# Optimization experiments

Hardware: AMD Instinct MI355X
Metric: run time of the kernel (lower is better)

## Reference

```python
import jax, jax.numpy as jnp
import numpy as np

B, N, FIN, FOUT, OPD = 2048, 64, 96, 128, 48
EPS = 1e-5      # nn.LayerNorm default eps
SLOPE = 0.01    # F.leaky_relu default negative_slope (used in GAT forward)


def setup_inputs() -> dict:
    key = jax.random.key(0)
    ks = jax.random.split(key, 12)
    stdv = 1.0 / np.sqrt(FOUT)
    h = jax.random.normal(ks[0], (B, N, FIN), jnp.float32)
    # binary DAG-style adjacency (float mask, as used multiplicatively in torch)
    adj = (jax.random.uniform(ks[1], (B, N, N)) < 0.3).astype(jnp.float32)
    op_emb = jax.random.normal(ks[2], (B, N, OPD), jnp.float32)
    # DenseGraphFlow params (uniform(-stdv, stdv) per reset_parameters)
    W = jax.random.uniform(ks[3], (FIN, FOUT), jnp.float32, -stdv, stdv)
    b = jax.random.uniform(ks[4], (FOUT,), jnp.float32, -stdv, stdv)
    Wop_d = jax.random.normal(ks[5], (OPD, FOUT), jnp.float32) * 0.05
    bop_d = jnp.zeros((FOUT,), jnp.float32)
    # GraphAttentionLayer params
    Wk = jax.random.normal(ks[6], (FIN, FOUT), jnp.float32) * 0.05
    a_w = jax.random.normal(ks[7], (FOUT,), jnp.float32) * 0.05
    Wop_g = jax.random.normal(ks[8], (OPD, FOUT), jnp.float32) * 0.05
    bop_g = jnp.zeros((FOUT,), jnp.float32)
    gamma = jnp.ones((FOUT,), jnp.float32)
    beta = jnp.zeros((FOUT,), jnp.float32)
    return dict(h=h, adj=adj, op_emb=op_emb, W=W, b=b, Wop_d=Wop_d, bop_d=bop_d,
                Wk=Wk, a_w=a_w, Wop_g=Wop_g, bop_g=bop_g, gamma=gamma, beta=beta)


def reference(h, adj, op_emb, W, b, Wop_d, bop_d, Wk, a_w, Wop_g, bop_g, gamma, beta):
    # ---- DenseGraphFlow (residual=True, opattention=True) ----
    support = jnp.einsum('bnf,fo->bno', h, W)                       # [B,N,FOUT]
    gate_d = jax.nn.sigmoid(op_emb @ Wop_d + bop_d)                 # [B,N,FOUT]
    dense = gate_d * jnp.einsum('bij,bjo->bio', adj, support) + support + b

    # ---- GraphAttentionLayer (unique_attn_proj=False -> Wq=Wv=Wk) ----
    Whk = jnp.einsum('bnf,fo->bno', h, Wk)                          # [B,N,FOUT]
    # torch builds a_input[b,i,j,m] = Whk[b,j,m] * Whk[b,i,m], then projects with
    # a (Linear FOUT->1). Exactly equivalent factored form (no [B,N,N,F] tensor):
    scores = jnp.einsum('bim,bjm->bij', Whk * a_w, Whk)             # [B,N,N]
    alpha = jnp.where(scores >= 0, scores, SLOPE * scores) * adj    # leaky_relu then adj mask
    attn = jax.nn.softmax(alpha, axis=-1)                           # softmax over j (torch dim=-2 of [b,i,j,1])
    hp = jnp.einsum('bij,bjo->bio', attn, Whk)                      # aggregate values
    gate_g = jax.nn.sigmoid(op_emb @ Wop_g + bop_g)
    hp = gate_g * hp
    # LayerNorm over last dim
    mu = jnp.mean(hp, axis=-1, keepdims=True)
    var = jnp.var(hp, axis=-1, keepdims=True)
    hp = (hp - mu) / jnp.sqrt(var + EPS) * gamma + beta

    # ---- ensemble combine ----
    return (dense + hp) / 2
```

## Files before the change

kernel.cpp:

```cpp
#include <hip/hip_runtime.h>

#define NB 2048
#define NN 64
#define KFIN 96
#define KFOUT 128
#define KOPD 48

typedef __attribute__((ext_vector_type(8))) short bf8;
typedef __attribute__((ext_vector_type(4))) float f32x4;
typedef __attribute__((ext_vector_type(4))) unsigned short us4;

__device__ __forceinline__ unsigned short f2bf(float f) {
  unsigned int u = __builtin_bit_cast(unsigned int, f);
  u += 0x7fffu + ((u >> 16) & 1u);
  return (unsigned short)(u >> 16);
}
__device__ __forceinline__ float bf2f(unsigned short s) {
  unsigned int u = ((unsigned int)s) << 16;
  return __builtin_bit_cast(float, u);
}
__device__ __forceinline__ us4 pack4(float a, float b, float c, float d) {
  us4 q; q.x = f2bf(a); q.y = f2bf(b); q.z = f2bf(c); q.w = f2bf(d); return q;
}

__global__ void prep_weights(const float* __restrict__ W, const float* __restrict__ Wk,
                             const float* __restrict__ Wd, const float* __restrict__ Wg,
                             unsigned short* __restrict__ ws) {
  int idx = blockIdx.x * 256 + threadIdx.x;
  if (idx >= 40960) return;
  float v;
  if (idx < 12288)      { int o = idx / 96, f = idx % 96; v = W[f * 128 + o]; }
  else if (idx < 24576) { int r = idx - 12288; int o = r / 96, f = r % 96; v = Wk[f * 128 + o]; }
  else if (idx < 32768) { int r = idx - 24576; int o = r >> 6, k = r & 63; v = (k < 48) ? Wd[k * 128 + o] : 0.f; }
  else                  { int r = idx - 32768; int o = r >> 6, k = r & 63; v = (k < 48) ? Wg[k * 128 + o] : 0.f; }
  ws[idx] = f2bf(v);
}

__global__ __launch_bounds__(256, 2) void gin_fused(
    const float* __restrict__ hg, const float* __restrict__ adjg,
    const float* __restrict__ opeg, const float* __restrict__ bvec,
    const float* __restrict__ bopd, const float* __restrict__ bopg,
    const float* __restrict__ awv, const float* __restrict__ gmv,
    const float* __restrict__ btv, const unsigned short* __restrict__ ws,
    float* __restrict__ out) {
  __shared__ __align__(16) char smem[50176];
  unsigned short* h_s   = (unsigned short*)smem;
  unsigned short* ope_s = (unsigned short*)(smem + 13312);
  unsigned short* adj_s = (unsigned short*)(smem + 22528);
  unsigned short* supT  = (unsigned short*)(smem + 31744);
  unsigned short* whkT  = (unsigned short*)smem;
  unsigned short* whk   = supT;

  const int t  = threadIdx.x;
  const int b  = blockIdx.x;
  const int w  = t >> 6;
  const int l  = t & 63;
  const int lr = l & 15;
  const int lg = l >> 4;
  const int kcol = 8 * lg;
  const int arow = w * 16 + lr;

  {
    const float4* p = (const float4*)(hg + (size_t)b * (NN * KFIN));
    #pragma unroll
    for (int i = 0; i < 6; ++i) {
      int idx = t + i * 256;
      float4 v = p[idx];
      int e = idx * 4, r = e / 96, c = e - r * 96;
      *(us4*)(h_s + r * 104 + c) = pack4(v.x, v.y, v.z, v.w);
    }
    const float4* pa = (const float4*)(adjg + (size_t)b * (NN * NN));
    #pragma unroll
    for (int i = 0; i < 4; ++i) {
      int idx = t + i * 256;
      float4 v = pa[idx];
      int e = idx * 4, r = e >> 6, c = e & 63;
      *(us4*)(adj_s + r * 72 + c) = pack4(v.x, v.y, v.z, v.w);
    }
    const float4* po = (const float4*)(opeg + (size_t)b * (NN * KOPD));
    #pragma unroll
    for (int i = 0; i < 3; ++i) {
      int idx = t + i * 256;
      float4 v = po[idx];
      int e = idx * 4, r = e / 48, c = e - r * 48;
      *(us4*)(ope_s + r * 72 + c) = pack4(v.x, v.y, v.z, v.w);
    }
    us4 z; z.x = 0; z.y = 0; z.z = 0; z.w = 0;
    *(us4*)(ope_s + (t >> 2) * 72 + 48 + (t & 3) * 4) = z;
  }
  __syncthreads();

  const unsigned short* WT  = ws;
  const unsigned short* WkT = ws + 12288;
  const unsigned short* WdT = ws + 24576;
  const unsigned short* WgT = ws + 32768;
  f32x4 zz = {0.f, 0.f, 0.f, 0.f};

  f32x4 sacc[8] = {zz, zz, zz, zz, zz, zz, zz, zz};
  #pragma unroll
  for (int kb = 0; kb < 3; ++kb) {
    bf8 a = *(const bf8*)(h_s + arow * 104 + kb * 32 + kcol);
    #pragma unroll
    for (int nb = 0; nb < 8; ++nb) {
      bf8 bb = *(const bf8*)(WT + (nb * 16 + lr) * 96 + kb * 32 + kcol);
      sacc[nb] = __builtin_amdgcn_mfma_f32_16x16x32_bf16(a, bb, sacc[nb], 0, 0, 0);
    }
  }
  #pragma unroll
  for (int nb = 0; nb < 8; ++nb)
    *(us4*)(supT + (nb * 16 + lr) * 72 + w * 16 + lg * 4) =
        pack4(sacc[nb][0], sacc[nb][1], sacc[nb][2], sacc[nb][3]);

  f32x4 gd[8] = {zz, zz, zz, zz, zz, zz, zz, zz};
  #pragma unroll
  for (int kb = 0; kb < 2; ++kb) {
    bf8 a = *(const bf8*)(ope_s + arow * 72 + kb * 32 + kcol);
    #pragma unroll
    for (int nb = 0; nb < 8; ++nb) {
      bf8 bb = *(const bf8*)(WdT + (nb * 16 + lr) * 64 + kb * 32 + kcol);
      gd[nb] = __builtin_amdgcn_mfma_f32_16x16x32_bf16(a, bb, gd[nb], 0, 0, 0);
    }
  }
  #pragma unroll
  for (int nb = 0; nb < 8; ++nb) {
    float bo = bopd[nb * 16 + lr];
    #pragma unroll
    for (int r = 0; r < 4; ++r) gd[nb][r] = 1.f / (1.f + __expf(-(gd[nb][r] + bo)));
  }
  __syncthreads();

  {
    f32x4 dacc[8] = {zz, zz, zz, zz, zz, zz, zz, zz};
    #pragma unroll
    for (int kb = 0; kb < 2; ++kb) {
      bf8 a = *(const bf8*)(adj_s + arow * 72 + kb * 32 + kcol);
      #pragma unroll
      for (int nb = 0; nb < 8; ++nb) {
        bf8 bb = *(const bf8*)(supT + (nb * 16 + lr) * 72 + kb * 32 + kcol);
        dacc[nb] = __builtin_amdgcn_mfma_f32_16x16x32_bf16(a, bb, dacc[nb], 0, 0, 0);
      }
    }
    #pragma unroll
    for (int nb = 0; nb < 8; ++nb) {
      float bc = bvec[nb * 16 + lr];
      #pragma unroll
      for (int r = 0; r < 4; ++r)
        sacc[nb][r] = gd[nb][r] * dacc[nb][r] + sacc[nb][r] + bc;
    }
  }

  f32x4 wacc[8] = {zz, zz, zz, zz, zz, zz, zz, zz};
  #pragma unroll
  for (int kb = 0; kb < 3; ++kb) {
    bf8 a = *(const bf8*)(h_s + arow * 104 + kb * 32 + kcol);
    #pragma unroll
    for (int nb = 0; nb < 8; ++nb) {
      bf8 bb = *(const bf8*)(WkT + (nb * 16 + lr) * 96 + kb * 32 + kcol);
      wacc[nb] = __builtin_amdgcn_mfma_f32_16x16x32_bf16(a, bb, wacc[nb], 0, 0, 0);
    }
  }

  f32x4 gg[8] = {zz, zz, zz, zz, zz, zz, zz, zz};
  #pragma unroll
  for (int kb = 0; kb < 2; ++kb) {
    bf8 a = *(const bf8*)(ope_s + arow * 72 + kb * 32 + kcol);
    #pragma unroll
    for (int nb = 0; nb < 8; ++nb) {
      bf8 bb = *(const bf8*)(WgT + (nb * 16 + lr) * 64 + kb * 32 + kcol);
      gg[nb] = __builtin_amdgcn_mfma_f32_16x16x32_bf16(a, bb, gg[nb], 0, 0, 0);
    }
  }
  #pragma unroll
  for (int nb = 0; nb < 8; ++nb) {
    float bo = bopg[nb * 16 + lr];
    #pragma unroll
    for (int r = 0; r < 4; ++r) gg[nb][r] = 1.f / (1.f + __expf(-(gg[nb][r] + bo)));
  }
  __syncthreads();

  #pragma unroll
  for (int nb = 0; nb < 8; ++nb) {
    int o = nb * 16 + lr;
    *(us4*)(whkT + o * 72 + w * 16 + lg * 4) =
        pack4(wacc[nb][0], wacc[nb][1], wacc[nb][2], wacc[nb][3]);
    #pragma unroll
    for (int r = 0; r < 4; ++r)
      whk[(w * 16 + lg * 4 + r) * 136 + o] = f2bf(wacc[nb][r]);
  }
  __syncthreads();

  f32x4 sc[4] = {zz, zz, zz, zz};
  #pragma unroll
  for (int kb = 0; kb < 4; ++kb) {
    bf8 ar = *(const bf8*)(whk + arow * 136 + kb * 32 + kcol);
    const float4* ap = (const float4*)(awv + kb * 32 + kcol);
    float4 a0 = ap[0], a1 = ap[1];
    bf8 a;
    a[0] = (short)f2bf(bf2f((unsigned short)ar[0]) * a0.x);
    a[1] = (short)f2bf(bf2f((unsigned short)ar[1]) * a0.y);
    a[2] = (short)f2bf(bf2f((unsigned short)ar[2]) * a0.z);
    a[3] = (short)f2bf(bf2f((unsigned short)ar[3]) * a0.w);
    a[4] = (short)f2bf(bf2f((unsigned short)ar[4]) * a1.x);
    a[5] = (short)f2bf(bf2f((unsigned short)ar[5]) * a1.y);
    a[6] = (short)f2bf(bf2f((unsigned short)ar[6]) * a1.z);
    a[7] = (short)f2bf(bf2f((unsigned short)ar[7]) * a1.w);
    #pragma unroll
    for (int jb = 0; jb < 4; ++jb) {
      bf8 bb = *(const bf8*)(whk + (jb * 16 + lr) * 136 + kb * 32 + kcol);
      sc[jb] = __builtin_amdgcn_mfma_f32_16x16x32_bf16(a, bb, sc[jb], 0, 0, 0);
    }
  }

  const int rowb = w * 16 + lg * 4;
  float al[4][4];
  #pragma unroll
  for (int jb = 0; jb < 4; ++jb)
    #pragma unroll
    for (int r = 0; r < 4; ++r) {
      float s = sc[jb][r];
      float am = bf2f(adj_s[(rowb + r) * 72 + jb * 16 + lr]);
      al[jb][r] = (s >= 0.f ? s : 0.01f * s) * am;
    }
  #pragma unroll
  for (int r = 0; r < 4; ++r) {
    float m = fmaxf(fmaxf(al[0][r], al[1][r]), fmaxf(al[2][r], al[3][r]));
    m = fmaxf(m, __shfl_xor(m, 1));
    m = fmaxf(m, __shfl_xor(m, 2));
    m = fmaxf(m, __shfl_xor(m, 4));
    m = fmaxf(m, __shfl_xor(m, 8));
    float s0 = 0.f;
    #pragma unroll
    for (int jb = 0; jb < 4; ++jb) { float p = __expf(al[jb][r] - m); al[jb][r] = p; s0 += p; }
    s0 += __shfl_xor(s0, 1);
    s0 += __shfl_xor(s0, 2);
    s0 += __shfl_xor(s0, 4);
    s0 += __shfl_xor(s0, 8);
    float inv = 1.f / s0;
    #pragma unroll
    for (int jb = 0; jb < 4; ++jb) al[jb][r] *= inv;
  }
  #pragma unroll
  for (int jb = 0; jb < 4; ++jb)
    #pragma unroll
    for (int r = 0; r < 4; ++r)
      adj_s[(rowb + r) * 72 + jb * 16 + lr] = f2bf(al[jb][r]);

  f32x4 hpacc[8] = {zz, zz, zz, zz, zz, zz, zz, zz};
  #pragma unroll
  for (int kb = 0; kb < 2; ++kb) {
    bf8 a = *(const bf8*)(adj_s + arow * 72 + kb * 32 + kcol);
    #pragma unroll
    for (int nb = 0; nb < 8; ++nb) {
      bf8 bb = *(const bf8*)(whkT + (nb * 16 + lr) * 72 + kb * 32 + kcol);
      hpacc[nb] = __builtin_amdgcn_mfma_f32_16x16x32_bf16(a, bb, hpacc[nb], 0, 0, 0);
    }
  }

  float gam[8], bet[8];
  #pragma unroll
  for (int nb = 0; nb < 8; ++nb) { gam[nb] = gmv[nb * 16 + lr]; bet[nb] = btv[nb * 16 + lr]; }
  float* outp = out + (size_t)b * (NN * KFOUT);
  #pragma unroll
  for (int r = 0; r < 4; ++r) {
    float hv[8]; float su = 0.f, sq = 0.f;
    #pragma unroll
    for (int nb = 0; nb < 8; ++nb) {
      float v = gg[nb][r] * hpacc[nb][r];
      hv[nb] = v; su += v; sq += v * v;
    }
    su += __shfl_xor(su, 1); su += __shfl_xor(su, 2);
    su += __shfl_xor(su, 4); su += __shfl_xor(su, 8);
    sq += __shfl_xor(sq, 1); sq += __shfl_xor(sq, 2);
    sq += __shfl_xor(sq, 4); sq += __shfl_xor(sq, 8);
    float mean = su * (1.f / 128.f);
    float var  = sq * (1.f / 128.f) - mean * mean;
    float rinv = rsqrtf(var + 1e-5f);
    int row = rowb + r;
    #pragma unroll
    for (int nb = 0; nb < 8; ++nb) {
      float hn = (hv[nb] - mean) * rinv * gam[nb] + bet[nb];
      outp[row * 128 + nb * 16 + lr] = (sacc[nb][r] + hn) * 0.5f;
    }
  }
}

extern "C" void kernel_launch(void* const* d_in, const int* in_sizes, int n_in,
                              void* d_out, int out_size, void* d_ws, size_t ws_size,
                              hipStream_t stream) {
  const float* h     = (const float*)d_in[0];
  const float* adj   = (const float*)d_in[1];
  const float* ope   = (const float*)d_in[2];
  const float* W     = (const float*)d_in[3];
  const float* bvec  = (const float*)d_in[4];
  const float* Wopd  = (const float*)d_in[5];
  const float* bopd  = (const float*)d_in[6];
  const float* Wk    = (const float*)d_in[7];
  const float* a_w   = (const float*)d_in[8];
  const float* Wopg  = (const float*)d_in[9];
  const float* bopg  = (const float*)d_in[10];
  const float* gamma = (const float*)d_in[11];
  const float* beta  = (const float*)d_in[12];
  float* out = (float*)d_out;
  unsigned short* ws = (unsigned short*)d_ws;

  prep_weights<<<dim3(160), dim3(256), 0, stream>>>(W, Wk, Wopd, Wopg, ws);
  gin_fused<<<dim3(NB), dim3(256), 0, stream>>>(h, adj, ope, bvec, bopd, bopg,
                                                a_w, gamma, beta, ws, out);
}
```

Before: 110.4 us.

## Load MFMA A-operands directly to registers and shrink LDS for higher occupancy

Result: slower. 153.1 us (+38.8%).

```diff
diff --git a/kernel.cpp b/kernel.cpp
--- a/kernel.cpp
+++ b/kernel.cpp
@@ -21,6 +21,18 @@
 }
 __device__ __forceinline__ us4 pack4(float a, float b, float c, float d) {
   us4 q; q.x = f2bf(a); q.y = f2bf(b); q.z = f2bf(c); q.w = f2bf(d); return q;
+}
+__device__ __forceinline__ bf8 pk8(float4 a, float4 b) {
+  bf8 r;
+  r[0] = (short)f2bf(a.x); r[1] = (short)f2bf(a.y); r[2] = (short)f2bf(a.z); r[3] = (short)f2bf(a.w);
+  r[4] = (short)f2bf(b.x); r[5] = (short)f2bf(b.y); r[6] = (short)f2bf(b.z); r[7] = (short)f2bf(b.w);
+  return r;
+}
+__device__ __forceinline__ unsigned int pk2(float lo, float hi) {
+  return (unsigned int)f2bf(lo) | ((unsigned int)f2bf(hi) << 16);
+}
+__device__ __forceinline__ float unpk(unsigned int p, int hi) {
+  return bf2f((unsigned short)(hi ? (p >> 16) : (p & 0xffffu)));
 }
 
 __global__ void prep_weights(const float* __restrict__ W, const float* __restrict__ Wk,
@@ -36,20 +48,19 @@
   ws[idx] = f2bf(v);
 }
 
-__global__ __launch_bounds__(256, 2) void gin_fused(
+#define LD1 68
+#define LD2 132
+#define LDA 68
+__global__ __launch_bounds__(256, 4) void gin_fused(
     const float* __restrict__ hg, const float* __restrict__ adjg,
     const float* __restrict__ opeg, const float* __restrict__ bvec,
     const float* __restrict__ bopd, const float* __restrict__ bopg,
     const float* __restrict__ awv, const float* __restrict__ gmv,
     const float* __restrict__ btv, const unsigned short* __restrict__ ws,
     float* __restrict__ out) {
-  __shared__ __align__(16) char smem[50176];
-  unsigned short* h_s   = (unsigned short*)smem;
-  unsigned short* ope_s = (unsigned short*)(smem + 13312);
-  unsigned short* adj_s = (unsigned short*)(smem + 22528);
-  unsigned short* supT  = (unsigned short*)(smem + 31744);
-  unsigned short* whkT  = (unsigned short*)smem;
-  unsigned short* whk   = supT;
+  __shared__ __align__(16) char smem[34304];
+  unsigned short* buf1 = (unsigned short*)smem;
+  unsigned short* buf2 = (unsigned short*)(smem + 17408);
 
   const int t  = threadIdx.x;
   const int b  = blockIdx.x;
@@ -59,36 +70,38 @@
   const int lg = l >> 4;
   const int kcol = 8 * lg;
   const int arow = w * 16 + lr;
-
+  const int rowb = w * 16 + lg * 4;
+
+  const float* hrow = hg   + (size_t)b * (NN * KFIN)  + arow * KFIN;
+  const float* orow = opeg + (size_t)b * (NN * KOPD)  + arow * KOPD;
+  const float* ajr  = adjg + (size_t)b * (NN * NN)    + arow * NN;
+
+  bf8 ha[3], oa[2], aa[2];
+  #pragma unroll
+  for (int kb = 0; kb < 3; ++kb) {
+    float4 p0 = *(const float4*)(hrow + kb * 32 + kcol);
+    float4 p1 = *(const float4*)(hrow + kb * 32 + kcol + 4);
+    ha[kb] = pk8(p0, p1);
+  }
   {
-    const float4* p = (const float4*)(hg + (size_t)b * (NN * KFIN));
-    #pragma unroll
-    for (int i = 0; i < 6; ++i) {
-      int idx = t + i * 256;
-      float4 v = p[idx];
-      int e = idx * 4, r = e / 96, c = e - r * 96;
-      *(us4*)(h_s + r * 104 + c) = pack4(v.x, v.y, v.z, v.w);
-    }
-    const float4* pa = (const float4*)(adjg + (size_t)b * (NN * NN));
-    #pragma unroll
-    for (int i = 0; i < 4; ++i) {
-      int idx = t + i * 256;
-      float4 v = pa[idx];
-      int e = idx * 4, r = e >> 6, c = e & 63;
-      *(us4*)(adj_s + r * 72 + c) = pack4(v.x, v.y, v.z, v.w);
-    }
-    const float4* po = (const float4*)(opeg + (size_t)b * (NN * KOPD));
-    #pragma unroll
-    for (int i = 0; i < 3; ++i) {
-      int idx = t + i * 256;
-      float4 v = po[idx];
-      int e = idx * 4, r = e / 48, c = e - r * 48;
-      *(us4*)(ope_s + r * 72 + c) = pack4(v.x, v.y, v.z, v.w);
-    }
-    us4 z; z.x = 0; z.y = 0; z.z = 0; z.w = 0;
-    *(us4*)(ope_s + (t >> 2) * 72 + 48 + (t & 3) * 4) = z;
-  }
-  __syncthreads();
+    float4 p0 = *(const float4*)(orow + kcol);
+    float4 p1 = *(const float4*)(orow + kcol + 4);
+    oa[0] = pk8(p0, p1);
+    if (lg < 2) {
+      float4 q0 = *(const float4*)(orow + 32 + kcol);
+      float4 q1 = *(const float4*)(orow + 32 + kcol + 4);
+      oa[1] = pk8(q0, q1);
+    } else {
+      bf8 z = {0, 0, 0, 0, 0, 0, 0, 0};
+      oa[1] = z;
+    }
+  }
+  #pragma unroll
+  for (int kb = 0; kb < 2; ++kb) {
+    float4 p0 = *(const float4*)(ajr + kb * 32 + kcol);
+    float4 p1 = *(const float4*)(ajr + kb * 32 + kcol + 4);
+    aa[kb] = pk8(p0, p1);
+  }
 
   const unsigned short* WT  = ws;
   const unsigned short* WkT = ws + 12288;
@@ -99,100 +112,113 @@
   f32x4 sacc[8] = {zz, zz, zz, zz, zz, zz, zz, zz};
   #pragma unroll
   for (int kb = 0; kb < 3; ++kb) {
-    bf8 a = *(const bf8*)(h_s + arow * 104 + kb * 32 + kcol);
     #pragma unroll
     for (int nb = 0; nb < 8; ++nb) {
       bf8 bb = *(const bf8*)(WT + (nb * 16 + lr) * 96 + kb * 32 + kcol);
-      sacc[nb] = __builtin_amdgcn_mfma_f32_16x16x32_bf16(a, bb, sacc[nb], 0, 0, 0);
+      sacc[nb] = __builtin_amdgcn_mfma_f32_16x16x32_bf16(ha[kb], bb, sacc[nb], 0, 0, 0);
     }
   }
   #pragma unroll
   for (int nb = 0; nb < 8; ++nb)
-    *(us4*)(supT + (nb * 16 + lr) * 72 + w * 16 + lg * 4) =
+    *(us4*)(buf1 + (nb * 16 + lr) * LD1 + w * 16 + lg * 4) =
         pack4(sacc[nb][0], sacc[nb][1], sacc[nb][2], sacc[nb][3]);
 
-  f32x4 gd[8] = {zz, zz, zz, zz, zz, zz, zz, zz};
-  #pragma unroll
-  for (int kb = 0; kb < 2; ++kb) {
-    bf8 a = *(const bf8*)(ope_s + arow * 72 + kb * 32 + kcol);
-    #pragma unroll
-    for (int nb = 0; nb < 8; ++nb) {
-      bf8 bb = *(const bf8*)(WdT + (nb * 16 + lr) * 64 + kb * 32 + kcol);
-      gd[nb] = __builtin_amdgcn_mfma_f32_16x16x32_bf16(a, bb, gd[nb], 0, 0, 0);
-    }
-  }
-  #pragma unroll
-  for (int nb = 0; nb < 8; ++nb) {
-    float bo = bopd[nb * 16 + lr];
-    #pragma unroll
-    for (int r = 0; r < 4; ++r) gd[nb][r] = 1.f / (1.f + __expf(-(gd[nb][r] + bo)));
-  }
-  __syncthreads();
-
+  unsigned int gdp[8][2];
   {
-    f32x4 dacc[8] = {zz, zz, zz, zz, zz, zz, zz, zz};
+    f32x4 gd[8] = {zz, zz, zz, zz, zz, zz, zz, zz};
     #pragma unroll
     for (int kb = 0; kb < 2; ++kb) {
-      bf8 a = *(const bf8*)(adj_s + arow * 72 + kb * 32 + kcol);
       #pragma unroll
       for (int nb = 0; nb < 8; ++nb) {
-        bf8 bb = *(const bf8*)(supT + (nb * 16 + lr) * 72 + kb * 32 + kcol);
-        dacc[nb] = __builtin_amdgcn_mfma_f32_16x16x32_bf16(a, bb, dacc[nb], 0, 0, 0);
+        bf8 bb = *(const bf8*)(WdT + (nb * 16 + lr) * 64 + kb * 32 + kcol);
+        gd[nb] = __builtin_amdgcn_mfma_f32_16x16x32_bf16(oa[kb], bb, gd[nb], 0, 0, 0);
       }
     }
     #pragma unroll
     for (int nb = 0; nb < 8; ++nb) {
-      float bc = bvec[nb * 16 + lr];
-      #pragma unroll
-      for (int r = 0; r < 4; ++r)
-        sacc[nb][r] = gd[nb][r] * dacc[nb][r] + sacc[nb][r] + bc;
-    }
+      float bo = bopd[nb * 16 + lr];
+      float g0 = 1.f / (1.f + __expf(-(gd[nb][0] + bo)));
+      float g1 = 1.f / (1.f + __expf(-(gd[nb][1] + bo)));
+      float g2 = 1.f / (1.f + __expf(-(gd[nb][2] + bo)));
+      float g3 = 1.f / (1.f + __expf(-(gd[nb][3] + bo)));
+      gdp[nb][0] = pk2(g0, g1); gdp[nb][1] = pk2(g2, g3);
+    }
+  }
+  __syncthreads();
+
+  unsigned int dnp[8][2];
+  #pragma unroll
+  for (int nb = 0; nb < 8; ++nb) {
+    f32x4 dacc = zz;
+    #pragma unroll
+    for (int kb = 0; kb < 2; ++kb) {
+      bf8 bb = *(const bf8*)(buf1 + (nb * 16 + lr) * LD1 + kb * 32 + kcol);
+      dacc = __builtin_amdgcn_mfma_f32_16x16x32_bf16(aa[kb], bb, dacc, 0, 0, 0);
+    }
+    float bc = bvec[nb * 16 + lr];
+    float d0 = unpk(gdp[nb][0], 0) * dacc[0] + sacc[nb][0] + bc;
+    float d1 = unpk(gdp[nb][0], 1) * dacc[1] + sacc[nb][1] + bc;
+    float d2 = unpk(gdp[nb][1], 0) * dacc[2] + sacc[nb][2] + bc;
+    float d3 = unpk(gdp[nb][1], 1) * dacc[3] + sacc[nb][3] + bc;
+    dnp[nb][0] = pk2(d0, d1); dnp[nb][1] = pk2(d2, d3);
   }
 
   f32x4 wacc[8] = {zz, zz, zz, zz, zz, zz, zz, zz};
   #pragma unroll
   for (int kb = 0; kb < 3; ++kb) {
-    bf8 a = *(const bf8*)(h_s + arow * 104 + kb * 32 + kcol);
     #pragma unroll
     for (int nb = 0; nb < 8; ++nb) {
       bf8 bb = *(const bf8*)(WkT + (nb * 16 + lr) * 96 + kb * 32 + kcol);
-      wacc[nb] = __builtin_amdgcn_mfma_f32_16x16x32_bf16(a, bb, wacc[nb], 0, 0, 0);
-    }
-  }
-
-  f32x4 gg[8] = {zz, zz, zz, zz, zz, zz, zz, zz};
-  #pragma unroll
-  for (int kb = 0; kb < 2; ++kb) {
-    bf8 a = *(const bf8*)(ope_s + arow * 72 + kb * 32 + kcol);
-    #pragma unroll
-    for (int nb = 0; nb < 8; ++nb) {
-      bf8 bb = *(const bf8*)(WgT + (nb * 16 + lr) * 64 + kb * 32 + kcol);
-      gg[nb] = __builtin_amdgcn_mfma_f32_16x16x32_bf16(a, bb, gg[nb], 0, 0, 0);
-    }
-  }
-  #pragma unroll
-  for (int nb = 0; nb < 8; ++nb) {
-    float bo = bopg[nb * 16 + lr];
-    #pragma unroll
-    for (int r = 0; r < 4; ++r) gg[nb][r] = 1.f / (1.f + __expf(-(gg[nb][r] + bo)));
+      wacc[nb] = __builtin_amdgcn_mfma_f32_16x16x32_bf16(ha[kb], bb, wacc[nb], 0, 0, 0);
+    }
   }
   __syncthreads();
 
   #pragma unroll
   for (int nb = 0; nb < 8; ++nb) {
     int o = nb * 16 + lr;
-    *(us4*)(whkT + o * 72 + w * 16 + lg * 4) =
+    *(us4*)(buf1 + o * LD1 + w * 16 + lg * 4) =
         pack4(wacc[nb][0], wacc[nb][1], wacc[nb][2], wacc[nb][3]);
     #pragma unroll
     for (int r = 0; r < 4; ++r)
-      whk[(w * 16 + lg * 4 + r) * 136 + o] = f2bf(wacc[nb][r]);
-  }
+      buf2[(w * 16 + lg * 4 + r) * LD2 + o] = f2bf(wacc[nb][r]);
+  }
+
+  unsigned int ggp[8][2];
+  {
+    f32x4 gg[8] = {zz, zz, zz, zz, zz, zz, zz, zz};
+    #pragma unroll
+    for (int kb = 0; kb < 2; ++kb) {
+      #pragma unroll
+      for (int nb = 0; nb < 8; ++nb) {
+        bf8 bb = *(const bf8*)(WgT + (nb * 16 + lr) * 64 + kb * 32 + kcol);
+        gg[nb] = __builtin_amdgcn_mfma_f32_16x16x32_bf16(oa[kb], bb, gg[nb], 0, 0, 0);
+      }
+    }
+    #pragma unroll
+    for (int nb = 0; nb < 8; ++nb) {
+      float bo = bopg[nb * 16 + lr];
+      float g0 = 1.f / (1.f + __expf(-(gg[nb][0] + bo)));
+      float g1 = 1.f / (1.f + __expf(-(gg[nb][1] + bo)));
+      float g2 = 1.f / (1.f + __expf(-(gg[nb][2] + bo)));
+      float g3 = 1.f / (1.f + __expf(-(gg[nb][3] + bo)));
+      ggp[nb][0] = pk2(g0, g1); ggp[nb][1] = pk2(g2, g3);
+    }
+  }
+
+  float msk[4][4];
+  #pragma unroll
+  for (int jb = 0; jb < 4; ++jb)
+    #pragma unroll
+    for (int r = 0; r < 4; ++r)
+      msk[jb][r] = adjg[(size_t)b * (NN * NN) + (rowb + r) * NN + jb * 16 + lr];
+
   __syncthreads();
 
   f32x4 sc[4] = {zz, zz, zz, zz};
   #pragma unroll
   for (int kb = 0; kb < 4; ++kb) {
-    bf8 ar = *(const bf8*)(whk + arow * 136 + kb * 32 + kcol);
+    bf8 ar = *(const bf8*)(buf2 + arow * LD2 + kb * 32 + kcol);
     const float4* ap = (const float4*)(awv + kb * 32 + kcol);
     float4 a0 = ap[0], a1 = ap[1];
     bf8 a;
@@ -206,20 +232,18 @@
     a[7] = (short)f2bf(bf2f((unsigned short)ar[7]) * a1.w);
     #pragma unroll
     for (int jb = 0; jb < 4; ++jb) {
-      bf8 bb = *(const bf8*)(whk + (jb * 16 + lr) * 136 + kb * 32 + kcol);
+      bf8 bb = *(const bf8*)(buf2 + (jb * 16 + lr) * LD2 + kb * 32 + kcol);
       sc[jb] = __builtin_amdgcn_mfma_f32_16x16x32_bf16(a, bb, sc[jb], 0, 0, 0);
     }
   }
 
-  const int rowb = w * 16 + lg * 4;
   float al[4][4];
   #pragma unroll
   for (int jb = 0; jb < 4; ++jb)
     #pragma unroll
     for (int r = 0; r < 4; ++r) {
       float s = sc[jb][r];
-      float am = bf2f(adj_s[(rowb + r) * 72 + jb * 16 + lr]);
-      al[jb][r] = (s >= 0.f ? s : 0.01f * s) * am;
+      al[jb][r] = (s >= 0.f ? s : 0.01f * s) * msk[jb][r];
     }
   #pragma unroll
   for (int r = 0; r < 4; ++r) {
@@ -239,19 +263,22 @@
     #pragma unroll
     for (int jb = 0; jb < 4; ++jb) al[jb][r] *= inv;
   }
+  __syncthreads();
+
+  unsigned short* attn_s = buf2;
   #pragma unroll
   for (int jb = 0; jb < 4; ++jb)
     #pragma unroll
     for (int r = 0; r < 4; ++r)
-      adj_s[(rowb + r) * 72 + jb * 16 + lr] = f2bf(al[jb][r]);
+      attn_s[(rowb + r) * LDA + jb * 16 + lr] = f2bf(al[jb][r]);
 
   f32x4 hpacc[8] = {zz, zz, zz, zz, zz, zz, zz, zz};
   #pragma unroll
   for (int kb = 0; kb < 2; ++kb) {
-    bf8 a = *(const bf8*)(adj_s + arow * 72 + kb * 32 + kcol);
-    #pragma unroll
-    for (int nb = 0; nb < 8; ++nb) {
-      bf8 bb = *(const bf8*)(whkT + (nb * 16 + lr) * 72 + kb * 32 + kcol);
+    bf8 a = *(const bf8*)(attn_s + arow * LDA + kb * 32 + kcol);
+    #pragma unroll
+    for (int nb = 0; nb < 8; ++nb) {
+      bf8 bb = *(const bf8*)(buf1 + (nb * 16 + lr) * LD1 + kb * 32 + kcol);
       hpacc[nb] = __builtin_amdgcn_mfma_f32_16x16x32_bf16(a, bb, hpacc[nb], 0, 0, 0);
     }
   }
@@ -265,7 +292,7 @@
     float hv[8]; float su = 0.f, sq = 0.f;
     #pragma unroll
     for (int nb = 0; nb < 8; ++nb) {
-      float v = gg[nb][r] * hpacc[nb][r];
+      float v = unpk(ggp[nb][r >> 1], r & 1) * hpacc[nb][r];
       hv[nb] = v; su += v; sq += v * v;
     }
     su += __shfl_xor(su, 1); su += __shfl_xor(su, 2);
@@ -279,7 +306,8 @@
     #pragma unroll
     for (int nb = 0; nb < 8; ++nb) {
       float hn = (hv[nb] - mean) * rinv * gam[nb] + bet[nb];
-      outp[row * 128 + nb * 16 + lr] = (sacc[nb][r] + hn) * 0.5f;
+      float dv = unpk(dnp[nb][r >> 1], r & 1);
+      outp[row * 128 + nb * 16 + lr] = (dv + hn) * 0.5f;
     }
   }
 }
```
